# Kernel tuning notes

Measured on AMD Instinct MI355X. Metric: run time of the kernel, lower is better.

Reference implementation:

```python
import jax, jax.numpy as jnp
import numpy as np

B, P, T = 32, 196, 32           # batch, num pixels (14*14), seq_len
E, H, A, V = 512, 512, 256, 30000  # embed, hidden, attention, vocab
FEAT = 2048

def _ln(x, g, b, eps=1e-5):
    m = jnp.mean(x, -1, keepdims=True)
    v = jnp.mean((x - m) ** 2, -1, keepdims=True)
    return (x - m) / jnp.sqrt(v + eps) * g + b

def setup_inputs() -> dict:
    key = jax.random.key(0)
    ks = iter(jax.random.split(key, 32))
    def rn(shape, s=0.05):
        return (jax.random.normal(next(ks), shape, dtype=jnp.float32) * s)
    inp = {
        'features': jax.random.normal(next(ks), (B, P, FEAT), dtype=jnp.float32),
        'captions': jax.random.randint(next(ks), (B, T), 0, V),
        # feature adapter Linear(2048->E) + LayerNorm
        'Wad': rn((E, FEAT)), 'bad': jnp.zeros((E,), jnp.float32),
        'g_ad': jnp.ones((E,), jnp.float32), 'b_ad': jnp.zeros((E,), jnp.float32),
        # additive attention
        'We': rn((A, E)), 'be': jnp.zeros((A,), jnp.float32),
        'Wd': rn((A, H)), 'bd': jnp.zeros((A,), jnp.float32),
        'Wf': rn((1, A)), 'bf': jnp.zeros((1,), jnp.float32),
        # embedding table (uniform(-0.1,0.1) as in torch init)
        'emb': jax.random.uniform(next(ks), (V, E), jnp.float32, -0.1, 0.1),
        # LSTM layer 0: input 2E, layer 1: input H; gates order i,f,g,o; forget bias 1
        'W_ih0': rn((4 * H, 2 * E)), 'W_hh0': rn((4 * H, H)),
        'b_ih0': jnp.concatenate([jnp.zeros(H), jnp.ones(H), jnp.zeros(2 * H)]).astype(jnp.float32),
        'b_hh0': jnp.zeros((4 * H,), jnp.float32),
        'W_ih1': rn((4 * H, H)), 'W_hh1': rn((4 * H, H)),
        'b_ih1': jnp.concatenate([jnp.zeros(H), jnp.ones(H), jnp.zeros(2 * H)]).astype(jnp.float32),
        'b_hh1': jnp.zeros((4 * H,), jnp.float32),
        # output head
        'W1': rn((H // 2, H)), 'b1': jnp.zeros((H // 2,), jnp.float32),
        'g1': jnp.ones((H // 2,), jnp.float32), 'bb1': jnp.zeros((H // 2,), jnp.float32),
        'W2': rn((V, H // 2)), 'b2': jnp.zeros((V,), jnp.float32),
    }
    return inp

def reference(features, captions, Wad, bad, g_ad, b_ad, We, be, Wd, bd, Wf, bf,
              emb, W_ih0, W_hh0, b_ih0, b_hh0, W_ih1, W_hh1, b_ih1, b_hh1,
              W1, b1, g1, bb1, W2, b2):
    # feature adapter (dropout = identity in eval)
    enc = _ln(jax.nn.relu(features @ Wad.T + bad), g_ad, b_ad)   # [B,P,E]
    att1 = enc @ We.T + be                                        # [B,P,A] (same every step)
    embs = emb[captions]                                          # [B,T,E]

    def lstm_cell(x, h, c, Wih, Whh, bih, bhh):
        gates = x @ Wih.T + bih + h @ Whh.T + bhh                 # [B,4H]
        i, f, g, o = jnp.split(gates, 4, axis=1)
        c_n = jax.nn.sigmoid(f) * c + jax.nn.sigmoid(i) * jnp.tanh(g)
        h_n = jax.nn.sigmoid(o) * jnp.tanh(c_n)
        return h_n, c_n

    def step(carry, emb_t):
        h, c = carry                                              # each [2,B,H]
        # additive attention against top-layer hidden state
        att2 = h[1] @ Wd.T + bd                                   # [B,A]
        e = (jax.nn.relu(att1 + att2[:, None, :]) @ Wf.T + bf)[..., 0]  # [B,P]
        alpha = jax.nn.softmax(e, axis=1)                         # (max-subtract is folded in)
        ctx = jnp.einsum('bp,bpe->be', alpha, enc)                # [B,E]
        x = jnp.concatenate([emb_t, ctx], axis=1)                 # [B,2E]
        h0, c0 = lstm_cell(x,  h[0], c[0], W_ih0, W_hh0, b_ih0, b_hh0)
        h1, c1 = lstm_cell(h0, h[1], c[1], W_ih1, W_hh1, b_ih1, b_hh1)
        out = jax.nn.relu(_ln(h1 @ W1.T + b1, g1, bb1))
        out = jnp.clip(out @ W2.T + b2, -10.0, 10.0)              # [B,V]
        return (jnp.stack([h0, h1]), jnp.stack([c0, c1])), out

    h0 = jnp.zeros((2, B, H), jnp.float32)
    c0 = jnp.zeros((2, B, H), jnp.float32)
    _, outs = jax.lax.scan(step, (h0, c0), jnp.swapaxes(embs, 0, 1))
    return jnp.swapaxes(outs, 0, 1)                               # [B,T,V]
```

## Files before the change

kernel.cpp:

```cpp
#include <hip/hip_runtime.h>

#define B_ 32
#define P_ 196
#define T_ 32
#define E_ 512
#define H_ 512
#define A_ 256
#define V_ 30000
#define FEAT_ 2048

typedef unsigned short u16;
typedef __attribute__((ext_vector_type(8))) short bf16x8;
typedef __attribute__((ext_vector_type(4))) float fx4;

#define MFMA16 __builtin_amdgcn_mfma_f32_16x16x32_bf16

__device__ __forceinline__ u16 f2b(float f){
  unsigned u = __builtin_bit_cast(unsigned, f);
  u += 0x7FFFu + ((u >> 16) & 1u);
  return (u16)(u >> 16);
}
__device__ __forceinline__ float b2f(u16 h){
  unsigned u = ((unsigned)h) << 16;
  return __builtin_bit_cast(float, u);
}
__device__ __forceinline__ float sigm(float x){ return 1.f/(1.f + __expf(-x)); }

#define PREP_BLOCKS 31670
__global__ void k_prep(const float* __restrict__ Wad, const float* __restrict__ We,
                       const float* __restrict__ W1f, const float* __restrict__ W2f,
                       const float* __restrict__ Wd,
                       const float* __restrict__ Wih0, const float* __restrict__ Whh0,
                       const float* __restrict__ Wih1, const float* __restrict__ Whh1,
                       const float* __restrict__ bih0, const float* __restrict__ bhh0,
                       const float* __restrict__ bih1, const float* __restrict__ bhh1,
                       const float* __restrict__ emb, const int* __restrict__ cap,
                       const float* __restrict__ feat,
                       u16* __restrict__ Wad16, u16* __restrict__ We16,
                       u16* __restrict__ W1_16, u16* __restrict__ W2pk,
                       unsigned* __restrict__ Wd2, u16* __restrict__ Wg0pk,
                       u16* __restrict__ W1ppk, float* __restrict__ bias0p,
                       float* __restrict__ bias1p, u16* __restrict__ embs16,
                       u16* __restrict__ fb16){
  int bid = blockIdx.x, tid = threadIdx.x;
  if (bid < 12288){
    int eid = bid*256 + tid;
    int j = eid & 7, l = (eid >> 3) & 63, frag = eid >> 9;
    int ks = frag % 12; int rest = frag / 12;
    int kw = rest & 3, q = (rest >> 2) & 3, s = rest >> 4;
    int n = q*512 + s*16 + (l & 15);
    int k = kw*384 + ks*32 + ((l >> 4) << 3) + j;
    float v = (k < 1024) ? Wih0[(size_t)n*1024 + k] : Whh0[(size_t)n*512 + (k - 1024)];
    Wg0pk[eid] = f2b(v);
  } else if (bid < 20480){
    int eid = (bid-12288)*256 + tid;
    int j = eid & 7, l = (eid >> 3) & 63, f = eid >> 9;
    int nf = f & 127, s = f >> 7;
    int np = nf*16 + (l & 15);
    int k = ((l >> 4) << 3) + j;
    int orig = ((np >> 4) & 3)*512 + (np >> 6)*16 + (np & 15);
    float v = (k < 16) ? Wih1[(size_t)orig*512 + s*16 + k]
                       : Whh1[(size_t)orig*512 + s*16 + (k - 16)];
    W1ppk[eid] = f2b(v);
  } else if (bid < 24230){
    int i = (bid-20480)*256 + tid;
    int l = i & 63, kc = (i >> 6) & 7, nf = i >> 9;
    int row = nf*16 + (l & 15);
    int col = kc*32 + (l >> 4)*8;
    const float4* s = (const float4*)(W2f + (size_t)row*256 + col);
    float4 a = s[0], b = s[1];
    ushort4* d = (ushort4*)(W2pk + (size_t)i*8);
    d[0] = make_ushort4(f2b(a.x), f2b(a.y), f2b(a.z), f2b(a.w));
    d[1] = make_ushort4(f2b(b.x), f2b(b.y), f2b(b.z), f2b(b.w));
  } else if (bid < 24742){
    int i = (bid-24230)*256 + tid;
    const float4* s = (const float4*)Wad + (size_t)i*2;
    float4 a = s[0], b = s[1];
    ushort4* d = (ushort4*)Wad16 + (size_t)i*2;
    d[0] = make_ushort4(f2b(a.x), f2b(a.y), f2b(a.z), f2b(a.w));
    d[1] = make_ushort4(f2b(b.x), f2b(b.y), f2b(b.z), f2b(b.w));
  } else if (bid < 24806){
    int i = (bid-24742)*256 + tid;
    const float4* s = (const float4*)We + (size_t)i*2;
    float4 a = s[0], b = s[1];
    ushort4* d = (ushort4*)We16 + (size_t)i*2;
    d[0] = make_ushort4(f2b(a.x), f2b(a.y), f2b(a.z), f2b(a.w));
    d[1] = make_ushort4(f2b(b.x), f2b(b.y), f2b(b.z), f2b(b.w));
  } else if (bid < 24870){
    int i = (bid-24806)*256 + tid;
    const float4* s = (const float4*)W1f + (size_t)i*2;
    float4 a = s[0], b = s[1];
    ushort4* d = (ushort4*)W1_16 + (size_t)i*2;
    d[0] = make_ushort4(f2b(a.x), f2b(a.y), f2b(a.z), f2b(a.w));
    d[1] = make_ushort4(f2b(b.x), f2b(b.y), f2b(b.z), f2b(b.w));
  } else if (bid < 25126){
    int i = (bid-24870)*256 + tid;
    int n = i & 255, kp = i >> 8;
    unsigned lo = f2b(Wd[n*512 + 2*kp]);
    unsigned hi = f2b(Wd[n*512 + 2*kp + 1]);
    Wd2[i] = lo | (hi << 16);
  } else if (bid < 25134){
    int n = (bid-25126)*256 + tid;
    int c = n & 15, q = (n >> 4) & 3, s = n >> 6;
    int orig = q*512 + s*16 + c;
    bias0p[n] = bih0[orig] + bhh0[orig];
  } else if (bid < 25142){
    int n = (bid-25134)*256 + tid;
    int c = n & 15, q = (n >> 4) & 3, s = n >> 6;
    int orig = q*512 + s*16 + c;
    bias1p[n] = bih1[orig] + bhh1[orig];
  } else if (bid < 25398){
    int r = (bid-25142)*4 + (tid >> 6), l = tid & 63;
    int t = r >> 5, b = r & 31;
    int c = cap[b*T_ + t];
    const float4* s = (const float4*)(emb + (size_t)c*E_) + l*2;
    float4 a = s[0], bb = s[1];
    ushort4* d = (ushort4*)(embs16 + (size_t)r*E_) + l*2;
    d[0] = make_ushort4(f2b(a.x), f2b(a.y), f2b(a.z), f2b(a.w));
    d[1] = make_ushort4(f2b(bb.x), f2b(bb.y), f2b(bb.z), f2b(bb.w));
  } else {
    int i = (bid-25398)*256 + tid;
    const float4* s = (const float4*)feat + (size_t)i*2;
    float4 a = s[0], b = s[1];
    ushort4* d = (ushort4*)fb16 + (size_t)i*2;
    d[0] = make_ushort4(f2b(a.x), f2b(a.y), f2b(a.z), f2b(a.w));
    d[1] = make_ushort4(f2b(b.x), f2b(b.y), f2b(b.z), f2b(b.w));
  }
}

template<int MODE, int BM, int BN, int KS, int NQ>
__launch_bounds__(256)
__global__ void k_gemm(const u16* __restrict__ A, const u16* __restrict__ W,
                       const float* __restrict__ bias, u16* __restrict__ outB,
                       int M, int N, int K){
  constexpr int NI = BN/32, MI = BM/32, SEGS = KS/8;
  __shared__ __align__(16) u16 As[BM][KS+8];
  __shared__ __align__(16) u16 Bs[BN][KS+8];
  int f = blockIdx.x;
  int p8 = f & 7; int rest = f >> 3;
  int q = rest % NQ; int pHigh = rest / NQ;
  int p = pHigh*8 + p8;
  if (p*BM >= M) return;
  int m0 = p*BM, n0 = q*BN;
  int tid = threadIdx.x;
  int l = tid & 63, w = tid >> 6;
  int wr = w >> 1, wc = w & 1;
  fx4 acc[MI][NI];
  #pragma unroll
  for (int i=0;i<MI;i++)
    #pragma unroll
    for (int j=0;j<NI;j++) acc[i][j] = (fx4){0.f,0.f,0.f,0.f};
  int lr = l & 15, lg = l >> 4;
  for (int k0 = 0; k0 < K; k0 += KS){
    #pragma unroll
    for (int it=0; it<BM*SEGS/256; ++it){
      int flat = it*256 + tid, rr = flat/SEGS, cs = (flat%SEGS)*8;
      *(uint4*)&As[rr][cs] = *(const uint4*)(A + (size_t)(m0+rr)*K + k0 + cs);
    }
    uint4 z = {0u,0u,0u,0u};
    #pragma unroll
    for (int it=0; it<BN*SEGS/256; ++it){
      int flat = it*256 + tid, rr = flat/SEGS, cs = (flat%SEGS)*8;
      int rb = n0 + rr;
      *(uint4*)&Bs[rr][cs] = (rb < N) ? *(const uint4*)(W + (size_t)rb*K + k0 + cs) : z;
    }
    __syncthreads();
    #pragma unroll
    for (int kk=0; kk<KS/32; ++kk){
      bf16x8 av[MI], bv[NI];
      #pragma unroll
      for (int mi=0; mi<MI; mi++) av[mi] = *(const bf16x8*)&As[wr*(BM/2) + mi*16 + lr][kk*32 + lg*8];
      #pragma unroll
      for (int ni=0; ni<NI; ni++) bv[ni] = *(const bf16x8*)&Bs[wc*(BN/2) + ni*16 + lr][kk*32 + lg*8];
      #pragma unroll
      for (int mi=0; mi<MI; mi++)
        #pragma unroll
        for (int ni=0; ni<NI; ni++)
          acc[mi][ni] = MFMA16(av[mi], bv[ni], acc[mi][ni], 0, 0, 0);
    }
    __syncthreads();
  }
  #pragma unroll
  for (int mi=0; mi<MI; mi++)
    #pragma unroll
    for (int ni=0; ni<NI; ni++){
      int col = n0 + wc*(BN/2) + ni*16 + lr;
      if (col >= N) continue;
      float bvs = bias[col];
      #pragma unroll
      for (int reg=0; reg<4; reg++){
        int rowm = m0 + wr*(BM/2) + mi*16 + lg*4 + reg;
        float v = acc[mi][ni][reg] + bvs;
        if (MODE == 0) v = fmaxf(v, 0.f);
        outB[(size_t)rowm*N + col] = f2b(v);
      }
    }
}

__global__ void k_ln1(const u16* __restrict__ pre, const float* __restrict__ g,
                      const float* __restrict__ bt, u16* __restrict__ enc){
  int row = blockIdx.x; int l = threadIdx.x;
  bf16x8 vv = *(const bf16x8*)(pre + (size_t)row*E_ + l*8);
  float x[8]; float s = 0.f;
  #pragma unroll
  for (int i=0;i<8;i++){ x[i] = b2f((u16)vv[i]); s += x[i]; }
  #pragma unroll
  for (int off=32; off; off>>=1) s += __shfl_xor(s, off, 64);
  float mean = s * (1.f/512.f);
  float vs = 0.f;
  #pragma unroll
  for (int i=0;i<8;i++){ float d = x[i]-mean; vs += d*d; }
  #pragma unroll
  for (int off=32; off; off>>=1) vs += __shfl_xor(vs, off, 64);
  float inv = rsqrtf(vs*(1.f/512.f) + 1e-5f);
  int c0 = l*8;
  u16 o[8];
  #pragma unroll
  for (int i=0;i<8;i++) o[i] = f2b((x[i]-mean)*inv*g[c0+i] + bt[c0+i]);
  ushort4* d = (ushort4*)(enc + (size_t)row*E_ + c0);
  d[0] = make_ushort4(o[0],o[1],o[2],o[3]);
  d[1] = make_ushort4(o[4],o[5],o[6],o[7]);
}

__device__ __forceinline__ void w1ln_block(const u16* __restrict__ h1all,
    const u16* __restrict__ W1, const float* __restrict__ b1,
    const float* __restrict__ g1v, const float* __restrict__ bb1,
    u16* __restrict__ hid, int u, int tid, float* red2, float* mv){
  int l = tid & 63, w = tid >> 6, lr = l & 15, lg = l >> 4;
  fx4 acc[2] = {{0,0,0,0},{0,0,0,0}};
  for (int k0 = 0; k0 < 512; k0 += 32){
    bf16x8 bv  = *(const bf16x8*)(W1 + (size_t)(w*16+lr)*512 + k0 + lg*8);
    bf16x8 av0 = *(const bf16x8*)(h1all + ((size_t)lr*T_ + u)*512 + k0 + lg*8);
    bf16x8 av1 = *(const bf16x8*)(h1all + ((size_t)(16+lr)*T_ + u)*512 + k0 + lg*8);
    acc[0] = MFMA16(av0, bv, acc[0], 0,0,0);
    acc[1] = MFMA16(av1, bv, acc[1], 0,0,0);
  }
  int col = w*16 + lr;
  float bc = b1[col];
  float val[2][4], s1[2][4], s2[2][4];
  #pragma unroll
  for (int mi=0;mi<2;mi++)
    #pragma unroll
    for (int reg=0;reg<4;reg++){
      float v = acc[mi][reg] + bc;
      val[mi][reg] = v; s1[mi][reg] = v; s2[mi][reg] = v*v;
    }
  #pragma unroll
  for (int off=1; off<16; off<<=1){
    #pragma unroll
    for (int mi=0;mi<2;mi++)
      #pragma unroll
      for (int reg=0;reg<4;reg++){
        s1[mi][reg] += __shfl_xor(s1[mi][reg], off, 64);
        s2[mi][reg] += __shfl_xor(s2[mi][reg], off, 64);
      }
  }
  if (lr == 0){
    #pragma unroll
    for (int mi=0;mi<2;mi++)
      #pragma unroll
      for (int reg=0;reg<4;reg++){
        int row = mi*16 + lg*4 + reg;
        red2[(0*16 + w)*32 + row] = s1[mi][reg];
        red2[(16   + w)*32 + row] = s2[mi][reg];
      }
  }
  __syncthreads();
  if (tid < 64){
    int which = tid >> 5, row = tid & 31;
    float s = 0.f;
    #pragma unroll
    for (int ww=0; ww<16; ++ww) s += red2[(which*16 + ww)*32 + row];
    mv[which*32 + row] = s;
  }
  __syncthreads();
  #pragma unroll
  for (int mi=0;mi<2;mi++)
    #pragma unroll
    for (int reg=0;reg<4;reg++){
      int row = mi*16 + lg*4 + reg;
      float mean = mv[row] * (1.f/256.f);
      float var  = mv[32+row] * (1.f/256.f) - mean*mean;
      float inv  = rsqrtf(var + 1e-5f);
      float o = fmaxf((val[mi][reg]-mean)*inv*g1v[col] + bb1[col], 0.f);
      hid[((size_t)u*32 + row)*256 + col] = f2b(o);
    }
}

__launch_bounds__(1024)
__global__ void k_w1(const u16* __restrict__ h1all, const u16* __restrict__ W1_16,
                     const float* __restrict__ b1, const float* __restrict__ g1v,
                     const float* __restrict__ bb1, u16* __restrict__ hid16){
  __shared__ float red2[1024];
  __shared__ float mv[64];
  w1ln_block(h1all, W1_16, b1, g1v, bb1, hid16, blockIdx.x, threadIdx.x, red2, mv);
}

__launch_bounds__(1024)
__global__ void k_head(const u16* __restrict__ hid, const u16* __restrict__ W2pk,
                       const float* __restrict__ b2, float* __restrict__ out){
  __shared__ __align__(16) union { u16 hA[32][264]; float Cs[32][260]; } S;
  int c = blockIdx.x, uh = blockIdx.y, tid = threadIdx.x;
  int l = tid & 63, w = tid >> 6, lr = l & 15, lg = l >> 4;
  int nf = c*16 + w;
  bool valid = nf < 1875;
  bf16x8 bw[8];
  if (valid){
    const u16* wp = W2pk + (size_t)nf*4096 + l*8;
    #pragma unroll
    for (int k0=0;k0<8;k0++) bw[k0] = *(const bf16x8*)(wp + k0*512);
  }
  int srow = tid >> 5, scc = (tid & 31)*8;
  int col0 = c*256 + scc;
  float bb[8];
  #pragma unroll
  for (int j=0;j<8;j++) bb[j] = (col0 + j < V_) ? b2[col0 + j] : 0.f;

  for (int ui=0; ui<16; ++ui){
    int u = uh*16 + ui;
    { int arow = tid >> 5, ak = (tid & 31)*8;
      *(uint4*)&S.hA[arow][ak] = *(const uint4*)(hid + ((size_t)u*32 + arow)*256 + ak); }
    __syncthreads();
    fx4 acc0 = {0,0,0,0}, acc1 = {0,0,0,0};
    if (valid){
      #pragma unroll
      for (int k0=0;k0<8;k0++){
        bf16x8 av0 = *(const bf16x8*)&S.hA[lr][k0*32 + lg*8];
        bf16x8 av1 = *(const bf16x8*)&S.hA[16+lr][k0*32 + lg*8];
        acc0 = MFMA16(av0, bw[k0], acc0, 0,0,0);
        acc1 = MFMA16(av1, bw[k0], acc1, 0,0,0);
      }
    }
    __syncthreads();
    #pragma unroll
    for (int reg=0; reg<4; ++reg){
      S.Cs[lg*4+reg][w*16+lr]    = acc0[reg];
      S.Cs[16+lg*4+reg][w*16+lr] = acc1[reg];
    }
    __syncthreads();
    if (col0 + 8 <= V_){
      float4 v0, v1;
      v0.x = fminf(fmaxf(S.Cs[srow][scc+0] + bb[0], -10.f), 10.f);
      v0.y = fminf(fmaxf(S.Cs[srow][scc+1] + bb[1], -10.f), 10.f);
      v0.z = fminf(fmaxf(S.Cs[srow][scc+2] + bb[2], -10.f), 10.f);
      v0.w = fminf(fmaxf(S.Cs[srow][scc+3] + bb[3], -10.f), 10.f);
      v1.x = fminf(fmaxf(S.Cs[srow][scc+4] + bb[4], -10.f), 10.f);
      v1.y = fminf(fmaxf(S.Cs[srow][scc+5] + bb[5], -10.f), 10.f);
      v1.z = fminf(fmaxf(S.Cs[srow][scc+6] + bb[6], -10.f), 10.f);
      v1.w = fminf(fmaxf(S.Cs[srow][scc+7] + bb[7], -10.f), 10.f);
      float* o = out + ((size_t)srow*T_ + u)*V_ + col0;
      *(float4*)o = v0; *(float4*)(o+4) = v1;
    }
    __syncthreads();
  }
}

__launch_bounds__(1024)
__global__ void k_ly(const float* __restrict__ part1, const float* __restrict__ bias1p,
                     float* __restrict__ c1buf, u16* __restrict__ h1all,
                     const unsigned* __restrict__ Wd2, const float* __restrict__ bd,
                     const u16* __restrict__ att1b, const u16* __restrict__ enc16,
                     const float* __restrict__ Wf, const float* __restrict__ bfp,
                     const u16* __restrict__ embs, u16* __restrict__ xh0cur, int t){
  int b = blockIdx.x, tid = threadIdx.x;
  int l = tid & 63, wid = tid >> 6;
  __shared__ float g1s[2048];
  __shared__ float h1s[512];
  __shared__ float a2p[4][256];
  __shared__ float a2[256], ev[256], red[8], wfv[256], bdv[256];
  __shared__ float cb[4][256][2];
  if (tid < 256){ wfv[tid] = Wf[tid]; bdv[tid] = bd[tid]; }
  float bf0 = bfp[0];

  if (t > 0){
    float acc0 = bias1p[tid], acc1 = bias1p[tid + 1024];
    #pragma unroll 4
    for (int s2=0; s2<32; ++s2){
      const float* pp = part1 + ((size_t)(s2*32 + b))*2048;
      acc0 += pp[tid];
      acc1 += pp[tid + 1024];
    }
    g1s[tid] = acc0; g1s[tid + 1024] = acc1;
    __syncthreads();
    if (tid < 512){
      int h = tid, s4 = h >> 4, c = h & 15, base = s4*64 + c;
      float gi = g1s[base], gf = g1s[base+16], gg = g1s[base+32], go = g1s[base+48];
      float cold = c1buf[b*512 + h];
      float cn = sigm(gf)*cold + sigm(gi)*tanhf(gg);
      c1buf[b*512 + h] = cn;
      float hn = sigm(go)*tanhf(cn);
      h1s[h] = hn;
      h1all[((size_t)b*T_ + (t-1))*512 + h] = f2b(hn);
    }
  } else {
    if (tid < 512) h1s[tid] = 0.f;
  }
  __syncthreads();
  if (t >= T_) return;

  {
    int n = tid & 255, kq = tid >> 8;
    float acc = 0.f;
    const unsigned* wp = Wd2 + (size_t)kq*64*256 + n;
    #pragma unroll 8
    for (int kp2 = 0; kp2 < 64; ++kp2){
      unsigned wv = wp[(size_t)kp2*256];
      int k0 = (kq*64 + kp2)*2;
      acc += h1s[k0]   * b2f((u16)(wv & 0xFFFFu))
           + h1s[k0+1] * b2f((u16)(wv >> 16));
    }
    a2p[kq][n] = acc;
  }
  __syncthreads();
  if (tid < 256) a2[tid] = a2p[0][tid] + a2p[1][tid] + a2p[2][tid] + a2p[3][tid] + bdv[tid];
  __syncthreads();
  for (int pi = 0; pi < 13; ++pi){
    int p = pi*16 + wid;
    if (p < P_){
      ushort4 av4 = *(const ushort4*)(att1b + (size_t)(b*P_ + p)*A_ + l*4);
      int j0 = l*4;
      float sum = fmaxf(b2f(av4.x)+a2[j0],  0.f)*wfv[j0]
                + fmaxf(b2f(av4.y)+a2[j0+1],0.f)*wfv[j0+1]
                + fmaxf(b2f(av4.z)+a2[j0+2],0.f)*wfv[j0+2]
                + fmaxf(b2f(av4.w)+a2[j0+3],0.f)*wfv[j0+3];
      #pragma unroll
      for (int off=32; off; off>>=1) sum += __shfl_xor(sum, off, 64);
      if (l == 0) ev[p] = sum + bf0;
    }
  }
  __syncthreads();
  if (tid < 256){
    float v = (tid < P_) ? ev[tid] : -1e30f;
    float m = v;
    #pragma unroll
    for (int off=32; off; off>>=1) m = fmaxf(m, __shfl_xor(m, off, 64));
    if (l == 0) red[wid] = m;
  }
  __syncthreads();
  float mg = fmaxf(fmaxf(red[0],red[1]), fmaxf(red[2],red[3]));
  if (tid < 256){
    float ex = (tid < P_) ? __expf(ev[tid] - mg) : 0.f;
    float ss = ex;
    #pragma unroll
    for (int off=32; off; off>>=1) ss += __shfl_xor(ss, off, 64);
    if (l == 0) red[4+wid] = ss;
    ev[tid] = ex;
  }
  __syncthreads();
  float inv = 1.f/(red[4]+red[5]+red[6]+red[7]);
  {
    int j = tid & 255, pq = tid >> 8;
    float A0 = 0.f, A1 = 0.f;
    const unsigned* ep = (const unsigned*)enc16 + ((size_t)b*P_ + pq*49)*256 + j;
    #pragma unroll 7
    for (int pi = 0; pi < 49; ++pi){
      unsigned vv = ep[(size_t)pi*256];
      float al = ev[pq*49 + pi];
      A0 += al * b2f((u16)(vv & 0xFFFFu));
      A1 += al * b2f((u16)(vv >> 16));
    }
    cb[pq][j][0] = A0; cb[pq][j][1] = A1;
  }
  __syncthreads();
  if (tid < 256){
    float c0 = (cb[0][tid][0]+cb[1][tid][0]+cb[2][tid][0]+cb[3][tid][0]) * inv;
    float c1 = (cb[0][tid][1]+cb[1][tid][1]+cb[2][tid][1]+cb[3][tid][1]) * inv;
    unsigned o = (unsigned)f2b(c0) | (((unsigned)f2b(c1)) << 16);
    *((unsigned*)(xh0cur + (size_t)b*1536 + 512) + tid) = o;
    ((unsigned*)(xh0cur + (size_t)b*1536))[tid] =
        ((const unsigned*)(embs + (size_t)(t*32+b)*E_))[tid];
  }
}

__launch_bounds__(1024)
__global__ void k_lx(const u16* __restrict__ xh0cur, u16* __restrict__ xh0nxt,
                     const u16* __restrict__ Wg0pk, const float* __restrict__ bias0p,
                     const u16* __restrict__ W1ppk, const u16* __restrict__ h1all,
                     float* __restrict__ c0buf, float* __restrict__ part1, int t){
  __shared__ float part[16][16][16];
  __shared__ float gsum[4][16][16];
  __shared__ __align__(16) u16 As[16][40];
  int tid = threadIdx.x;
  int s = blockIdx.x >> 1, half = blockIdx.x & 1;
  int l = tid & 63, kw = tid >> 6, lr = l & 15, lg = l >> 4;
  int babs = half*16 + lr;

  bf16x8 a[3];
  #pragma unroll
  for (int ks=0;ks<3;ks++)
    a[ks] = *(const bf16x8*)(xh0cur + (size_t)babs*1536 + kw*96 + ks*32 + lg*8);
  if (tid < 128){
    int bb = tid >> 3, kk = (tid & 7)*2;
    unsigned hv = 0;
    if (t > 0) hv = *(const unsigned*)(h1all + ((size_t)(half*16+bb)*T_ + (t-1))*512 + s*16 + kk);
    *(unsigned*)&As[bb][16+kk] = hv;
  }
  for (int q=0;q<4;q++){
    fx4 acc0 = (fx4){0,0,0,0};
    const u16* wp = Wg0pk + (size_t)(((s*4+q)*4 + (kw>>2))*12 + (kw&3)*3)*512 + l*8;
    #pragma unroll
    for (int ks=0;ks<3;ks++){
      bf16x8 bf8 = *(const bf16x8*)(wp + ks*512);
      acc0 = MFMA16(a[ks], bf8, acc0, 0,0,0);
    }
    #pragma unroll
    for (int reg=0;reg<4;reg++)
      part[kw][lg*4+reg][lr] = acc0[reg];
    __syncthreads();
    if (tid < 256){
      int bb = tid >> 4, c = tid & 15;
      float g = bias0p[s*64 + q*16 + c];
      #pragma unroll
      for (int kw2=0; kw2<16; ++kw2) g += part[kw2][bb][c];
      gsum[q][bb][c] = g;
    }
    __syncthreads();
  }
  if (tid < 256){
    int bb = tid >> 4, c = tid & 15;
    int h = s*16 + c, ba = half*16 + bb;
    float gi = gsum[0][bb][c], gf = gsum[1][bb][c], gg = gsum[2][bb][c], go = gsum[3][bb][c];
    float cold = c0buf[ba*512 + h];
    float cn = sigm(gf)*cold + sigm(gi)*tanhf(gg);
    c0buf[ba*512 + h] = cn;
    u16 hb = f2b(sigm(go)*tanhf(cn));
    xh0nxt[(size_t)ba*1536 + 1024 + h] = hb;
    As[bb][c] = hb;
  }
  __syncthreads();
  bf16x8 pa0 = *(const bf16x8*)&As[lr][lg*8];
  #pragma unroll 2
  for (int i=0;i<8;i++){
    int nf = kw*8 + i;
    bf16x8 bf8 = *(const bf16x8*)(W1ppk + (size_t)(s*128 + nf)*512 + l*8);
    fx4 A0 = MFMA16(pa0, bf8, (fx4){0,0,0,0}, 0,0,0);
    float* o = part1 + ((size_t)s*32 + half*16)*2048 + nf*16 + lr;
    #pragma unroll
    for (int reg=0;reg<4;reg++)
      o[(size_t)(lg*4+reg)*2048] = A0[reg];
  }
}

extern "C" void kernel_launch(void* const* d_in, const int* in_sizes, int n_in,
                              void* d_out, int out_size, void* d_ws, size_t ws_size,
                              hipStream_t stream){
  (void)in_sizes; (void)n_in; (void)out_size; (void)ws_size;
  const float* features = (const float*)d_in[0];
  const int*   captions = (const int*)d_in[1];
  const float* Wad  = (const float*)d_in[2];
  const float* bad  = (const float*)d_in[3];
  const float* g_ad = (const float*)d_in[4];
  const float* b_ad = (const float*)d_in[5];
  const float* We   = (const float*)d_in[6];
  const float* be   = (const float*)d_in[7];
  const float* Wd   = (const float*)d_in[8];
  const float* bd   = (const float*)d_in[9];
  const float* Wf   = (const float*)d_in[10];
  const float* bfp  = (const float*)d_in[11];
  const float* emb  = (const float*)d_in[12];
  const float* W_ih0 = (const float*)d_in[13];
  const float* W_hh0 = (const float*)d_in[14];
  const float* b_ih0 = (const float*)d_in[15];
  const float* b_hh0 = (const float*)d_in[16];
  const float* W_ih1 = (const float*)d_in[17];
  const float* W_hh1 = (const float*)d_in[18];
  const float* b_ih1 = (const float*)d_in[19];
  const float* b_hh1 = (const float*)d_in[20];
  const float* W1  = (const float*)d_in[21];
  const float* b1  = (const float*)d_in[22];
  const float* g1  = (const float*)d_in[23];
  const float* bb1 = (const float*)d_in[24];
  const float* W2  = (const float*)d_in[25];
  const float* b2  = (const float*)d_in[26];
  float* out = (float*)d_out;

  char* wsb = (char*)d_ws;
  size_t off = 0;
  auto alloc = [&](size_t bytes)->char*{
    char* p = wsb + off; off += (bytes + 255) & ~(size_t)255; return p;
  };
  u16* fb16    = (u16*)alloc((size_t)6272*2048*2);
  u16* Wad16   = (u16*)alloc((size_t)512*2048*2);
  u16* We16    = (u16*)alloc((size_t)256*512*2);
  u16* W1_16   = (u16*)alloc((size_t)256*512*2);
  u16* W2pk    = (u16*)alloc((size_t)1875*8*512*2);
  unsigned* Wd2 = (unsigned*)alloc((size_t)256*256*4);
  u16* Wg0pk   = (u16*)alloc((size_t)2048*1536*2);
  u16* W1ppk   = (u16*)alloc((size_t)32*128*512*2);
  float* bias0p = (float*)alloc(2048*4);
  float* bias1p = (float*)alloc(2048*4);
  u16* embs16  = (u16*)alloc((size_t)1024*512*2);
  u16* pre16   = (u16*)alloc((size_t)6272*512*2);
  u16* enc16   = (u16*)alloc((size_t)6272*512*2);
  u16* att1_16 = (u16*)alloc((size_t)6272*256*2);
  u16* xh0     = (u16*)alloc((size_t)2*32*1536*2);
  float* c0buf = (float*)alloc(32*512*4);
  float* c1buf = (float*)alloc(32*512*4);
  float* part1 = (float*)alloc((size_t)32*32*2048*4);
  u16* h1all16 = (u16*)alloc((size_t)1024*512*2);
  u16* hid16   = (u16*)alloc((size_t)1024*256*2);

  hipMemsetAsync(xh0, 0, 196608 + 65536 + 65536, stream);

  k_prep<<<PREP_BLOCKS,256,0,stream>>>(Wad, We, W1, W2, Wd,
                                       W_ih0, W_hh0, W_ih1, W_hh1,
                                       b_ih0, b_hh0, b_ih1, b_hh1,
                                       emb, captions, features,
                                       Wad16, We16, W1_16, W2pk, Wd2,
                                       Wg0pk, W1ppk, bias0p, bias1p, embs16, fb16);

  k_gemm<0,64,64,64,8><<<832,256,0,stream>>>(fb16, Wad16, bad, pre16, 6272, 512, 2048);
  k_ln1<<<6272,64,0,stream>>>(pre16, g_ad, b_ad, enc16);
  k_gemm<1,64,64,64,4><<<416,256,0,stream>>>(enc16, We16, be, att1_16, 6272, 256, 512);

  u16* xb[2] = { xh0, xh0 + 32*1536 };
  for (int t = 0; t < T_; ++t){
    k_ly<<<32,1024,0,stream>>>(part1, bias1p, c1buf, h1all16, Wd2, bd,
                               att1_16, enc16, Wf, bfp, embs16, xb[t&1], t);
    k_lx<<<64,1024,0,stream>>>(xb[t&1], xb[1-(t&1)], Wg0pk, bias0p,
                               W1ppk, h1all16, c0buf, part1, t);
  }
  k_ly<<<32,1024,0,stream>>>(part1, bias1p, c1buf, h1all16, Wd2, bd,
                             att1_16, enc16, Wf, bfp, embs16, xb[0], T_);

  k_w1<<<32,1024,0,stream>>>(h1all16, W1_16, b1, g1, bb1, hid16);
  k_head<<<dim3(118,2),1024,0,stream>>>(hid16, W2pk, b2, out);
}
```

Before: 1.244 ms.

## Split-K the feature adapter GEMM and reduce partials in LayerNorm kernel

Replaces the adapter GEMM (6272x512x2048) with a split-K variant that runs four K-slices across four times as many blocks and writes fp32 partial sums. The LayerNorm kernel now sums the four partials, adds the bias, applies ReLU and normalizes, which moves the epilogue out of the GEMM. The aim is more parallelism than the original 832 blocks give on this GPU. The cost is roughly 51 MB of extra fp32 partial writes and reads. It also raises an unroll factor in the per-step partial reduction loop.

After: 1.204 ms (median of 2 runs). 3.2% less time.

```diff
diff --git a/kernel.cpp b/kernel.cpp
--- a/kernel.cpp
+++ b/kernel.cpp
@@ -128,6 +128,72 @@
   }
 }
 
+template<int BM, int BN, int KS, int NQ, int NKQ>
+__launch_bounds__(256)
+__global__ void k_gemmSK(const u16* __restrict__ A, const u16* __restrict__ W,
+                         float* __restrict__ outP, int M, int N, int K){
+  constexpr int NI = BN/32, MI = BM/32, SEGS = KS/8;
+  __shared__ __align__(16) u16 As[BM][KS+8];
+  __shared__ __align__(16) u16 Bs[BN][KS+8];
+  int f = blockIdx.x;
+  int inner = 8*NQ*((M/BM + 7)/8);
+  int kq = f / inner; f %= inner;
+  int p8 = f & 7; int rest = f >> 3;
+  int q = rest % NQ; int pHigh = rest / NQ;
+  int p = pHigh*8 + p8;
+  if (p*BM >= M) return;
+  int m0 = p*BM, n0 = q*BN;
+  int kper = K / NKQ;
+  int kbeg = kq * kper, kend = kbeg + kper;
+  int tid = threadIdx.x;
+  int l = tid & 63, w = tid >> 6;
+  int wr = w >> 1, wc = w & 1;
+  fx4 acc[MI][NI];
+  #pragma unroll
+  for (int i=0;i<MI;i++)
+    #pragma unroll
+    for (int j=0;j<NI;j++) acc[i][j] = (fx4){0.f,0.f,0.f,0.f};
+  int lr = l & 15, lg = l >> 4;
+  for (int k0 = kbeg; k0 < kend; k0 += KS){
+    #pragma unroll
+    for (int it=0; it<BM*SEGS/256; ++it){
+      int flat = it*256 + tid, rr = flat/SEGS, cs = (flat%SEGS)*8;
+      *(uint4*)&As[rr][cs] = *(const uint4*)(A + (size_t)(m0+rr)*K + k0 + cs);
+    }
+    #pragma unroll
+    for (int it=0; it<BN*SEGS/256; ++it){
+      int flat = it*256 + tid, rr = flat/SEGS, cs = (flat%SEGS)*8;
+      *(uint4*)&Bs[rr][cs] = *(const uint4*)(W + (size_t)(n0+rr)*K + k0 + cs);
+    }
+    __syncthreads();
+    #pragma unroll
+    for (int kk=0; kk<KS/32; ++kk){
+      bf16x8 av[MI], bv[NI];
+      #pragma unroll
+      for (int mi=0; mi<MI; mi++) av[mi] = *(const bf16x8*)&As[wr*(BM/2) + mi*16 + lr][kk*32 + lg*8];
+      #pragma unroll
+      for (int ni=0; ni<NI; ni++) bv[ni] = *(const bf16x8*)&Bs[wc*(BN/2) + ni*16 + lr][kk*32 + lg*8];
+      #pragma unroll
+      for (int mi=0; mi<MI; mi++)
+        #pragma unroll
+        for (int ni=0; ni<NI; ni++)
+          acc[mi][ni] = MFMA16(av[mi], bv[ni], acc[mi][ni], 0, 0, 0);
+    }
+    __syncthreads();
+  }
+  #pragma unroll
+  for (int mi=0; mi<MI; mi++)
+    #pragma unroll
+    for (int ni=0; ni<NI; ni++){
+      int col = n0 + wc*(BN/2) + ni*16 + lr;
+      #pragma unroll
+      for (int reg=0; reg<4; reg++){
+        int rowm = m0 + wr*(BM/2) + mi*16 + lg*4 + reg;
+        outP[((size_t)kq*M + rowm)*N + col] = acc[mi][ni][reg];
+      }
+    }
+}
+
 template<int MODE, int BM, int BN, int KS, int NQ>
 __launch_bounds__(256)
 __global__ void k_gemm(const u16* __restrict__ A, const u16* __restrict__ W,
@@ -197,13 +263,29 @@
     }
 }
 
-__global__ void k_ln1(const u16* __restrict__ pre, const float* __restrict__ g,
-                      const float* __restrict__ bt, u16* __restrict__ enc){
+__global__ void k_ln1(const float* __restrict__ preP, const float* __restrict__ bad,
+                      const float* __restrict__ g, const float* __restrict__ bt,
+                      u16* __restrict__ enc){
   int row = blockIdx.x; int l = threadIdx.x;
-  bf16x8 vv = *(const bf16x8*)(pre + (size_t)row*E_ + l*8);
-  float x[8]; float s = 0.f;
-  #pragma unroll
-  for (int i=0;i<8;i++){ x[i] = b2f((u16)vv[i]); s += x[i]; }
+  int c0 = l*8;
+  float x[8];
+  {
+    const float4* p0 = (const float4*)(preP + ((size_t)0*6272 + row)*E_ + c0);
+    const float4* p1 = (const float4*)(preP + ((size_t)1*6272 + row)*E_ + c0);
+    const float4* p2 = (const float4*)(preP + ((size_t)2*6272 + row)*E_ + c0);
+    const float4* p3 = (const float4*)(preP + ((size_t)3*6272 + row)*E_ + c0);
+    float4 a0 = p0[0], b0 = p0[1];
+    float4 a1 = p1[0], b1 = p1[1];
+    float4 a2 = p2[0], b2 = p2[1];
+    float4 a3 = p3[0], b3 = p3[1];
+    x[0] = a0.x+a1.x+a2.x+a3.x; x[1] = a0.y+a1.y+a2.y+a3.y;
+    x[2] = a0.z+a1.z+a2.z+a3.z; x[3] = a0.w+a1.w+a2.w+a3.w;
+    x[4] = b0.x+b1.x+b2.x+b3.x; x[5] = b0.y+b1.y+b2.y+b3.y;
+    x[6] = b0.z+b1.z+b2.z+b3.z; x[7] = b0.w+b1.w+b2.w+b3.w;
+  }
+  float s = 0.f;
+  #pragma unroll
+  for (int i=0;i<8;i++){ x[i] = fmaxf(x[i] + bad[c0+i], 0.f); s += x[i]; }
   #pragma unroll
   for (int off=32; off; off>>=1) s += __shfl_xor(s, off, 64);
   float mean = s * (1.f/512.f);
@@ -213,7 +295,6 @@
   #pragma unroll
   for (int off=32; off; off>>=1) vs += __shfl_xor(vs, off, 64);
   float inv = rsqrtf(vs*(1.f/512.f) + 1e-5f);
-  int c0 = l*8;
   u16 o[8];
   #pragma unroll
   for (int i=0;i<8;i++) o[i] = f2b((x[i]-mean)*inv*g[c0+i] + bt[c0+i]);
@@ -374,7 +455,7 @@
 
   if (t > 0){
     float acc0 = bias1p[tid], acc1 = bias1p[tid + 1024];
-    #pragma unroll 4
+    #pragma unroll 8
     for (int s2=0; s2<32; ++s2){
       const float* pp = part1 + ((size_t)(s2*32 + b))*2048;
       acc0 += pp[tid];
@@ -590,7 +671,6 @@
   float* bias0p = (float*)alloc(2048*4);
   float* bias1p = (float*)alloc(2048*4);
   u16* embs16  = (u16*)alloc((size_t)1024*512*2);
-  u16* pre16   = (u16*)alloc((size_t)6272*512*2);
   u16* enc16   = (u16*)alloc((size_t)6272*512*2);
   u16* att1_16 = (u16*)alloc((size_t)6272*256*2);
   u16* xh0     = (u16*)alloc((size_t)2*32*1536*2);
@@ -599,6 +679,7 @@
   float* part1 = (float*)alloc((size_t)32*32*2048*4);
   u16* h1all16 = (u16*)alloc((size_t)1024*512*2);
   u16* hid16   = (u16*)alloc((size_t)1024*256*2);
+  float* pre32f = (float*)alloc((size_t)4*6272*512*4);
 
   hipMemsetAsync(xh0, 0, 196608 + 65536 + 65536, stream);
 
@@ -609,8 +690,8 @@
                                        Wad16, We16, W1_16, W2pk, Wd2,
                                        Wg0pk, W1ppk, bias0p, bias1p, embs16, fb16);
 
-  k_gemm<0,64,64,64,8><<<832,256,0,stream>>>(fb16, Wad16, bad, pre16, 6272, 512, 2048);
-  k_ln1<<<6272,64,0,stream>>>(pre16, g_ad, b_ad, enc16);
+  k_gemmSK<64,64,64,8,4><<<3328,256,0,stream>>>(fb16, Wad16, pre32f, 6272, 512, 2048);
+  k_ln1<<<6272,64,0,stream>>>(pre32f, bad, g_ad, b_ad, enc16);
   k_gemm<1,64,64,64,4><<<416,256,0,stream>>>(enc16, We16, be, att1_16, 6272, 256, 512);
 
   u16* xb[2] = { xh0, xh0 + 32*1536 };
```
